# Performance work log

Hardware: AMD Instinct MI355X
Metric: run time of the kernel (lower is better)

Reference implementation:

```python
import jax, jax.numpy as jnp
import numpy as np

N = 500000   # nodes per batched graph
D = 64       # per-graph node feature dim (encoded_dims // 2)
P = 1000000  # number of interface candidate pairs
ED = 2 * D   # encoded_dims = 128


def setup_inputs() -> dict:
    key = jax.random.key(0)
    k1, k2, k3, k4, k5, k6 = jax.random.split(key, 6)
    graph1_x = jax.random.normal(k1, (N, D), dtype=jnp.float32)
    graph2_x = jax.random.normal(k2, (N, D), dtype=jnp.float32)
    idx_left = jax.random.randint(k3, (P,), 0, N, dtype=jnp.int32).astype(jnp.int64)
    idx_right = jax.random.randint(k4, (P,), 0, N, dtype=jnp.int32).astype(jnp.int64)
    W1 = jax.random.normal(k5, (ED, ED), dtype=jnp.float32) * (1.0 / np.sqrt(ED))
    b1 = jnp.zeros((ED,), dtype=jnp.float32)
    W2 = jax.random.normal(k6, (1, ED), dtype=jnp.float32) * (1.0 / np.sqrt(ED))
    b2 = jnp.zeros((1,), dtype=jnp.float32)
    return {"graph1_x": graph1_x, "graph2_x": graph2_x,
            "idx_left": idx_left, "idx_right": idx_right,
            "W1": W1, "b1": b1, "W2": W2, "b2": b2}


def reference(graph1_x, graph2_x, idx_left, idx_right, W1, b1, W2, b2):
    # Gather interface node features from both encoded graphs.
    left = graph1_x[idx_left]    # [P, D]
    right = graph2_x[idx_right]  # [P, D]
    x = jnp.concatenate([left, right], axis=1)  # [P, 2D]
    # top_net: Linear -> ReLU -> Dropout(eval: identity) -> Linear
    h = jax.nn.relu(x @ W1.T + b1)  # [P, ED]
    out = h @ W2.T + b2             # [P, 1]
    return out
```

## Files before the change

kernel.cpp:

```cpp
#include <hip/hip_runtime.h>


typedef __bf16 bf16x8 __attribute__((ext_vector_type(8)));
typedef float f32x16 __attribute__((ext_vector_type(16)));

__device__ __forceinline__ unsigned f2bf(float f) {
  union { float f; unsigned u; } v;
  v.f = f;
  unsigned u = v.u;
  return (u + 0x7fffu + ((u >> 16) & 1u)) >> 16;
}

__global__ __launch_bounds__(256) void w1_frag_kernel(
    const float* __restrict__ W1, uint4* __restrict__ w1f) {
  int t = blockIdx.x * 256 + threadIdx.x;
  int lane = t & 63;
  int nt = (t >> 6) & 3;
  int ks = t >> 8;
  int n = lane & 31, h = lane >> 5;
  const float4* src =
      (const float4*)(W1 + ((nt * 32 + n) * 128 + ks * 16 + h * 8));
  float4 a = src[0], b = src[1];
  uint4 o;
  o.x = f2bf(a.x) | (f2bf(a.y) << 16);
  o.y = f2bf(a.z) | (f2bf(a.w) << 16);
  o.z = f2bf(b.x) | (f2bf(b.y) << 16);
  o.w = f2bf(b.z) | (f2bf(b.w) << 16);
  w1f[t] = o;
}

__global__ __launch_bounds__(256, 5) void pip_main_kernel(
    const float* __restrict__ g1, const float* __restrict__ g2,
    const int* __restrict__ il, const int* __restrict__ ir,
    const bf16x8* __restrict__ w1f,
    const float* __restrict__ b1, const float* __restrict__ w2,
    const float* __restrict__ b2,
    float* __restrict__ out, int P) {
  __shared__ unsigned char A[4][8192];

  const int t = threadIdx.x;
  const int lane = t & 63;
  const int w = t >> 6;
  const int pair0 = blockIdx.x * 128;

  const int sub = lane & 15;
  const int g = lane >> 4;
  const int side = g & 1;
  const int phalf = g >> 1;
  const float* feat = side ? g2 : g1;
  const int* idxarr = side ? ir : il;

  int idxv[16];
#pragma unroll
  for (int j = 0; j < 16; ++j) {
    int gp = pair0 + w * 32 + j * 2 + phalf;
    int pidx = (gp < P) ? gp : (P - 1);
    idxv[j] = idxarr[pidx];
  }

  unsigned char* Aw = &A[w][0];
#pragma unroll
  for (int j = 0; j < 16; ++j) {
    int pl = j * 2 + phalf;
    float4 v = *(const float4*)(feat + (size_t)idxv[j] * 64 + sub * 4);
    unsigned lo = f2bf(v.x) | (f2bf(v.y) << 16);
    unsigned hi = f2bf(v.z) | (f2bf(v.w) << 16);
    int g16 = side * 8 + (sub >> 1);
    *(uint2*)(Aw + pl * 256 + ((g16 ^ (pl & 7)) << 4) + ((sub & 1) << 3)) =
        make_uint2(lo, hi);
  }
  asm volatile("s_waitcnt lgkmcnt(0)" ::: "memory");

  const int n = lane & 31;
  const int h = lane >> 5;

  f32x16 acc[4];
#pragma unroll
  for (int nt = 0; nt < 4; ++nt)
#pragma unroll
    for (int i = 0; i < 16; ++i) acc[nt][i] = 0.0f;

  const unsigned char* Abase = Aw + n * 256;
  const int rk = n & 7;
#pragma unroll
  for (int ks = 0; ks < 8; ++ks) {
    bf16x8 af = *(const bf16x8*)(Abase + (((ks * 2 + h) ^ rk) << 4));
#pragma unroll
    for (int nt = 0; nt < 4; ++nt) {
      bf16x8 bfr = w1f[(ks * 4 + nt) * 64 + lane];
      acc[nt] = __builtin_amdgcn_mfma_f32_32x32x16_bf16(af, bfr, acc[nt], 0, 0, 0);
    }
  }

  float b1v[4], w2v[4];
#pragma unroll
  for (int nt = 0; nt < 4; ++nt) {
    b1v[nt] = b1[nt * 32 + n];
    w2v[nt] = w2[nt * 32 + n];
  }
  const float bias2 = b2[0];

#pragma unroll
  for (int r = 0; r < 16; ++r) {
    float s = 0.0f;
#pragma unroll
    for (int nt = 0; nt < 4; ++nt) {
      float v = acc[nt][r] + b1v[nt];
      v = fmaxf(v, 0.0f);
      s = fmaf(v, w2v[nt], s);
    }
    s += __shfl_xor(s, 1);
    s += __shfl_xor(s, 2);
    s += __shfl_xor(s, 4);
    s += __shfl_xor(s, 8);
    s += __shfl_xor(s, 16);
    if (n == 0) {
      int row = (r & 3) + 8 * (r >> 2) + 4 * h;
      int gp = pair0 + w * 32 + row;
      if (gp < P) out[gp] = s + bias2;
    }
  }
}

extern "C" void kernel_launch(void* const* d_in, const int* in_sizes, int n_in,
                              void* d_out, int out_size, void* d_ws, size_t ws_size,
                              hipStream_t stream) {
  const float* g1 = (const float*)d_in[0];
  const float* g2 = (const float*)d_in[1];
  const int* il = (const int*)d_in[2];
  const int* ir = (const int*)d_in[3];
  const float* W1 = (const float*)d_in[4];
  const float* b1 = (const float*)d_in[5];
  const float* w2 = (const float*)d_in[6];
  const float* b2 = (const float*)d_in[7];
  float* out = (float*)d_out;
  const int P = out_size;

  w1_frag_kernel<<<8, 256, 0, stream>>>(W1, (uint4*)d_ws);

  const int nblocks = (P + 127) / 128;
  pip_main_kernel<<<nblocks, 256, 0, stream>>>(
      g1, g2, il, ir, (const bf16x8*)d_ws, b1, w2, b2, out, P);
}
```

Before: 342.4 us.

## Batch gather loads in groups of eight and process MFMA N-tiles sequentially

The gather phase now issues eight independent float4 loads before converting and storing them to LDS, so more memory requests are in flight at once. The MFMA loop is reordered so each of the four N-tiles gets its own 16-register accumulator and is reduced into a running ReLU·w2 sum right away, replacing four live accumulators with one. Launch bounds drop from 5 to 4 waves per SIMD, giving the compiler more register room. The trade-off is lower occupancy and a serial dependency chain per tile, which overlaps MFMA work less.

```diff
diff --git a/kernel.cpp b/kernel.cpp
--- a/kernel.cpp
+++ b/kernel.cpp
@@ -29,7 +29,7 @@
   w1f[t] = o;
 }
 
-__global__ __launch_bounds__(256, 5) void pip_main_kernel(
+__global__ __launch_bounds__(256, 4) void pip_main_kernel(
     const float* __restrict__ g1, const float* __restrict__ g2,
     const int* __restrict__ il, const int* __restrict__ ir,
     const bf16x8* __restrict__ w1f,
@@ -59,56 +59,60 @@
   }
 
   unsigned char* Aw = &A[w][0];
+  const int g16 = side * 8 + (sub >> 1);
 #pragma unroll
-  for (int j = 0; j < 16; ++j) {
-    int pl = j * 2 + phalf;
-    float4 v = *(const float4*)(feat + (size_t)idxv[j] * 64 + sub * 4);
-    unsigned lo = f2bf(v.x) | (f2bf(v.y) << 16);
-    unsigned hi = f2bf(v.z) | (f2bf(v.w) << 16);
-    int g16 = side * 8 + (sub >> 1);
-    *(uint2*)(Aw + pl * 256 + ((g16 ^ (pl & 7)) << 4) + ((sub & 1) << 3)) =
-        make_uint2(lo, hi);
+  for (int b = 0; b < 2; ++b) {
+    float4 vv[8];
+#pragma unroll
+    for (int j = 0; j < 8; ++j) {
+      vv[j] =
+          *(const float4*)(feat + (size_t)idxv[b * 8 + j] * 64 + sub * 4);
+    }
+#pragma unroll
+    for (int j = 0; j < 8; ++j) {
+      int pl = (b * 8 + j) * 2 + phalf;
+      unsigned lo = f2bf(vv[j].x) | (f2bf(vv[j].y) << 16);
+      unsigned hi = f2bf(vv[j].z) | (f2bf(vv[j].w) << 16);
+      *(uint2*)(Aw + pl * 256 + ((g16 ^ (pl & 7)) << 4) + ((sub & 1) << 3)) =
+          make_uint2(lo, hi);
+    }
   }
   asm volatile("s_waitcnt lgkmcnt(0)" ::: "memory");
 
   const int n = lane & 31;
   const int h = lane >> 5;
 
-  f32x16 acc[4];
-#pragma unroll
-  for (int nt = 0; nt < 4; ++nt)
-#pragma unroll
-    for (int i = 0; i < 16; ++i) acc[nt][i] = 0.0f;
-
   const unsigned char* Abase = Aw + n * 256;
   const int rk = n & 7;
+
+  float sacc[16];
 #pragma unroll
-  for (int ks = 0; ks < 8; ++ks) {
-    bf16x8 af = *(const bf16x8*)(Abase + (((ks * 2 + h) ^ rk) << 4));
+  for (int i = 0; i < 16; ++i) sacc[i] = 0.0f;
+  const float bias2 = b2[0];
+
+#pragma unroll 1
+  for (int nt = 0; nt < 4; ++nt) {
+    const float b1v = b1[nt * 32 + n];
+    const float w2v = w2[nt * 32 + n];
+    f32x16 acc;
 #pragma unroll
-    for (int nt = 0; nt < 4; ++nt) {
+    for (int i = 0; i < 16; ++i) acc[i] = 0.0f;
+#pragma unroll
+    for (int ks = 0; ks < 8; ++ks) {
+      bf16x8 af = *(const bf16x8*)(Abase + (((ks * 2 + h) ^ rk) << 4));
       bf16x8 bfr = w1f[(ks * 4 + nt) * 64 + lane];
-      acc[nt] = __builtin_amdgcn_mfma_f32_32x32x16_bf16(af, bfr, acc[nt], 0, 0, 0);
+      acc = __builtin_amdgcn_mfma_f32_32x32x16_bf16(af, bfr, acc, 0, 0, 0);
+    }
+#pragma unroll
+    for (int r = 0; r < 16; ++r) {
+      float v = fmaxf(acc[r] + b1v, 0.0f);
+      sacc[r] = fmaf(v, w2v, sacc[r]);
     }
   }
 
-  float b1v[4], w2v[4];
-#pragma unroll
-  for (int nt = 0; nt < 4; ++nt) {
-    b1v[nt] = b1[nt * 32 + n];
-    w2v[nt] = w2[nt * 32 + n];
-  }
-  const float bias2 = b2[0];
-
 #pragma unroll
   for (int r = 0; r < 16; ++r) {
-    float s = 0.0f;
-#pragma unroll
-    for (int nt = 0; nt < 4; ++nt) {
-      float v = acc[nt][r] + b1v[nt];
-      v = fmaxf(v, 0.0f);
-      s = fmaf(v, w2v[nt], s);
-    }
+    float s = sacc[r];
     s += __shfl_xor(s, 1);
     s += __shfl_xor(s, 2);
     s += __shfl_xor(s, 4);
```

Result: no change. 343.3 us (+0.3%).
